# Kernel optimization log

Hardware: AMD Instinct MI355X
Metric: run time of the kernel (lower is better)

Reference implementation:

```python
import jax, jax.numpy as jnp
import numpy as np
import math

LAYER_NUMBER = 2          # coeff for query-key layer scaling
HEAD_DIM = 128
NORM_FACTOR = math.sqrt(HEAD_DIM) * LAYER_NUMBER  # apply_query_key_layer_scaling
COEFF = float(LAYER_NUMBER)
MASK_FILL = -10000.0


def setup_inputs() -> dict:
    key = jax.random.key(0)
    k1, k2, k3, k4 = jax.random.split(key, 4)
    sq, b, nh, hn = 2048, 2, 16, HEAD_DIM
    query_layer = jax.random.normal(k1, (sq, b, nh, hn), dtype=jnp.float32)
    key_layer = jax.random.normal(k2, (sq, b, nh, hn), dtype=jnp.float32)
    value_layer = jax.random.normal(k3, (sq, b, nh, hn), dtype=jnp.float32)
    attention_mask = jax.random.bernoulli(k4, 0.1, (b, 1, sq, sq))
    return {
        "query_layer": query_layer,
        "key_layer": key_layer,
        "value_layer": value_layer,
        "attention_mask": attention_mask,
    }


def reference(query_layer, key_layer, value_layer, attention_mask):
    sq, b, nh, hn = query_layer.shape
    # raw scores: QK^T / norm_factor  -> [b, h, sq, sk]
    scores = jnp.einsum("sbhd,tbhd->bhst", query_layer, key_layer) / NORM_FACTOR
    # MatchedScaleMaskSoftmax: scale by coeff (softmax in fp32), mask-fill, softmax
    x = scores * COEFF
    x = jnp.where(attention_mask, MASK_FILL, x)
    probs = jax.nn.softmax(x, axis=-1)
    # zero out rows where every key is masked
    all_k_masked = jnp.all(attention_mask, axis=-1)  # [b, 1, sq]
    probs = probs * (1.0 - all_k_masked.astype(probs.dtype))[..., None]
    # (dropout p=0.0 -> identity)
    # context: probs @ V -> [sq, b, h, hn] -> [sq, b, hidden]
    ctx = jnp.einsum("bhst,tbhd->sbhd", probs, value_layer)
    return ctx.reshape(sq, b, nh * hn)
```

## Files before the change

kernel.cpp:

```cpp
#include <hip/hip_runtime.h>
#include <math.h>

#define SQ   2048
#define DH   128
#define NKT  32
#define SCALEF 0.08838834764831845f
#define SHIFTF 16.0f

typedef __attribute__((ext_vector_type(8))) short bf16x8;
typedef __attribute__((ext_vector_type(4))) float f32x4;

__device__ __forceinline__ unsigned short f2b(float f) {
    unsigned int u = __float_as_uint(f);
    u += 0x7FFFu + ((u >> 16) & 1u);
    return (unsigned short)(u >> 16);
}

typedef __attribute__((address_space(1))) const unsigned int guint;
typedef __attribute__((address_space(3))) unsigned int luint;
__device__ __forceinline__ void load_lds16(const void* g, void* l) {
    __builtin_amdgcn_global_load_lds((guint*)g, (luint*)l, 16, 0, 0);
}


__global__ __launch_bounds__(256)
void prep_all(const float* __restrict__ K, const float* __restrict__ V,
              const int* __restrict__ M,
              unsigned short* __restrict__ Kp, unsigned short* __restrict__ Vp,
              unsigned long long* __restrict__ B)
{
    const int bid = blockIdx.x;
    const int tid = threadIdx.x;
    if (bid < 4096) {
        int id   = bid * 256 + tid;
        int quad = id & 3;
        int key  = (id >> 2) & 63;
        int ks   = (id >> 8) & 3;
        int kt   = (id >> 10) & 31;
        int bh   = id >> 15;
        const float* src = K + (size_t)(kt * 64 + key) * 4096 + bh * DH + ks * 32 + quad * 8;
        float4 f0 = *(const float4*)src;
        float4 f1 = *(const float4*)(src + 4);
        uint4 o;
        o.x = (unsigned)f2b(f0.x) | ((unsigned)f2b(f0.y) << 16);
        o.y = (unsigned)f2b(f0.z) | ((unsigned)f2b(f0.w) << 16);
        o.z = (unsigned)f2b(f1.x) | ((unsigned)f2b(f1.y) << 16);
        o.w = (unsigned)f2b(f1.z) | ((unsigned)f2b(f1.w) << 16);
        *(uint4*)(Kp + (size_t)id * 8) = o;
    } else if (bid < 5120) {
        int t  = bid - 4096;
        int kt = t & 31, bh = t >> 5;
        int d  = tid & 127;
        int hf = tid >> 7;
        const float* vb = V + (size_t)kt * 64 * 4096 + bh * DH + d;
        unsigned short* ob = Vp + (size_t)t * 8192 + (size_t)(hf * 128 + d) * 32;
        #pragma unroll
        for (int p = 0; p < 4; p++) {
            unsigned short v[8];
            #pragma unroll
            for (int j = 0; j < 8; j++)
                v[j] = f2b(vb[(size_t)(hf * 32 + p * 8 + j) * 4096]);
            uint4 o;
            o.x = (unsigned)v[0] | ((unsigned)v[1] << 16);
            o.y = (unsigned)v[2] | ((unsigned)v[3] << 16);
            o.z = (unsigned)v[4] | ((unsigned)v[5] << 16);
            o.w = (unsigned)v[6] | ((unsigned)v[7] << 16);
            *(uint4*)(ob + p * 8) = o;
        }
    } else {
        int b2   = bid - 5120;
        int wid  = b2 * 4 + (tid >> 6);
        int lane = tid & 63;
        const int* src = M + (size_t)wid * SQ + lane;
        unsigned long long* dst = B + (size_t)wid * NKT;
        for (int t = 0; t < NKT; t++) {
            unsigned long long bm = __ballot(src[t * 64] != 0);
            if (lane == 0) dst[t] = bm;
        }
    }
}

__global__ __launch_bounds__(256, 2)
void fa2(const float* __restrict__ Q, const unsigned short* __restrict__ Kp,
         const unsigned short* __restrict__ Vp, const unsigned long long* __restrict__ MB,
         float* __restrict__ out)
{
    __shared__ __align__(16) unsigned short K_lds[64 * 128];
    __shared__ __align__(16) unsigned short V_lds[64 * 128];
    __shared__ __align__(16) unsigned short P_lds[4 * 2048];

    const int tid  = threadIdx.x;
    const int w    = tid >> 6;
    const int lane = tid & 63;
    const int quad = lane >> 4;
    const int c    = lane & 15;

    const int bid = blockIdx.x;
    const int qt  = bid & 15;
    const int bh  = bid >> 4;
    const int b_i = bh >> 4;
    const int qbase = qt * 128 + w * 32;
    const size_t bh_off = (size_t)bh * DH;

    bf16x8 aq[2][4];
    #pragma unroll
    for (int blk = 0; blk < 2; blk++) {
        const float* qrow = Q + (size_t)(qbase + blk * 16 + c) * 4096 + bh_off;
        #pragma unroll
        for (int ks = 0; ks < 4; ks++) {
            const int d0 = ks * 32 + quad * 8;
            float4 f0 = *(const float4*)(qrow + d0);
            float4 f1 = *(const float4*)(qrow + d0 + 4);
            bf16x8 a;
            a[0] = (short)f2b(f0.x); a[1] = (short)f2b(f0.y);
            a[2] = (short)f2b(f0.z); a[3] = (short)f2b(f0.w);
            a[4] = (short)f2b(f1.x); a[5] = (short)f2b(f1.y);
            a[6] = (short)f2b(f1.z); a[7] = (short)f2b(f1.w);
            aq[blk][ks] = a;
        }
    }

    f32x4 oa[2][8];
    #pragma unroll
    for (int blk = 0; blk < 2; blk++)
        #pragma unroll
        for (int nb = 0; nb < 8; nb++) oa[blk][nb] = (f32x4){0.f, 0.f, 0.f, 0.f};
    float l[2][4];
    #pragma unroll
    for (int blk = 0; blk < 2; blk++)
        #pragma unroll
        for (int r = 0; r < 4; r++) l[blk][r] = 0.0f;

    const unsigned short* KpT = Kp + (size_t)bh * (NKT * 8192);
    const unsigned short* VpT = Vp + (size_t)bh * (NKT * 8192);
    const unsigned long long* mb0 = MB + (size_t)(b_i * SQ + qbase + quad * 4) * NKT;
    const unsigned long long* mb1 = mb0 + 16 * NKT;
    unsigned short* Pw = &P_lds[w * 2048];

    for (int kt = 0; kt < NKT; kt++) {
        __syncthreads();
        {
            const unsigned short* kg = KpT + (size_t)kt * 8192;
            const unsigned short* vg = VpT + (size_t)kt * 8192;
            #pragma unroll
            for (int i = 0; i < 4; i++) {
                int ch = w * 64 + i * 256;
                load_lds16(kg + (size_t)(ch + lane) * 8, &K_lds[ch * 8]);
            }
            #pragma unroll
            for (int i = 0; i < 4; i++) {
                int ch = w * 64 + i * 256;
                load_lds16(vg + (size_t)(ch + lane) * 8, &V_lds[ch * 8]);
            }
        }
        unsigned long long mrow[2][4];
        #pragma unroll
        for (int r = 0; r < 4; r++) {
            mrow[0][r] = mb0[r * NKT + kt];
            mrow[1][r] = mb1[r * NKT + kt];
        }
        __syncthreads();

        f32x4 s[2][4];
        #pragma unroll
        for (int blk = 0; blk < 2; blk++)
            #pragma unroll
            for (int nb = 0; nb < 4; nb++) s[blk][nb] = (f32x4){0.f, 0.f, 0.f, 0.f};
        #pragma unroll
        for (int nb = 0; nb < 4; nb++) {
            bf16x8 bk[4];
            #pragma unroll
            for (int ks = 0; ks < 4; ks++)
                bk[ks] = *(const bf16x8*)&K_lds[ks * 2048 + nb * 512 + c * 32 + quad * 8];
            #pragma unroll
            for (int blk = 0; blk < 2; blk++)
                #pragma unroll
                for (int ks = 0; ks < 4; ks++)
                    s[blk][nb] = __builtin_amdgcn_mfma_f32_16x16x32_bf16(aq[blk][ks], bk[ks], s[blk][nb], 0, 0, 0);
        }

        #pragma unroll
        for (int blk = 0; blk < 2; blk++) {
            #pragma unroll
            for (int r = 0; r < 4; r++) {
                unsigned long long bits = mrow[blk][r];
                #pragma unroll
                for (int nb = 0; nb < 4; nb++) {
                    float p = __expf(fmaf(s[blk][nb][r], SCALEF, -SHIFTF));
                    if ((unsigned)(bits >> (nb * 16 + c)) & 1u) p = 0.0f;
                    l[blk][r] += p;
                    int quad2 = (((nb & 1) * 2) + (c >> 3)) ^ quad;
                    Pw[(nb >> 1) * 1024 + blk * 512 + quad * 128 + r * 32 + quad2 * 8 + (c & 7)] = f2b(p);
                }
            }
        }

        bf16x8 ap[2][2];
        #pragma unroll
        for (int blk = 0; blk < 2; blk++)
            #pragma unroll
            for (int ks2 = 0; ks2 < 2; ks2++)
                ap[blk][ks2] = *(const bf16x8*)&Pw[ks2 * 1024 + blk * 512 + c * 32 + ((quad ^ (c >> 2)) * 8)];
        #pragma unroll
        for (int nb = 0; nb < 8; nb++) {
            bf16x8 bv0 = *(const bf16x8*)&V_lds[nb * 512 + c * 32 + quad * 8];
            bf16x8 bv1 = *(const bf16x8*)&V_lds[4096 + nb * 512 + c * 32 + quad * 8];
            #pragma unroll
            for (int blk = 0; blk < 2; blk++) {
                oa[blk][nb] = __builtin_amdgcn_mfma_f32_16x16x32_bf16(ap[blk][0], bv0, oa[blk][nb], 0, 0, 0);
                oa[blk][nb] = __builtin_amdgcn_mfma_f32_16x16x32_bf16(ap[blk][1], bv1, oa[blk][nb], 0, 0, 0);
            }
        }
    }

    #pragma unroll
    for (int blk = 0; blk < 2; blk++) {
        #pragma unroll
        for (int r = 0; r < 4; r++) {
            float t = l[blk][r];
            t += __shfl_xor(t, 1, 64);
            t += __shfl_xor(t, 2, 64);
            t += __shfl_xor(t, 4, 64);
            t += __shfl_xor(t, 8, 64);
            float inv = (t > 0.0f) ? (1.0f / t) : 0.0f;
            float* orow = out + (size_t)(qbase + blk * 16 + quad * 4 + r) * 4096 + bh_off;
            #pragma unroll
            for (int nb = 0; nb < 8; nb++)
                orow[nb * 16 + c] = oa[blk][nb][r] * inv;
        }
    }
}

__global__ __launch_bounds__(256)
void fa_fallback(const float* __restrict__ Q, const float* __restrict__ K,
                 const float* __restrict__ V, const int* __restrict__ mask,
                 float* __restrict__ out)
{
    __shared__ unsigned short K_lds[64 * 136];
    __shared__ unsigned short Vt_lds[128 * 72];
    __shared__ unsigned short P_lds[4 * 16 * 72];
    const int tid = threadIdx.x, w = tid >> 6, lane = tid & 63, quad = lane >> 4, c = lane & 15;
    const int gid = blockIdx.x, qtile = gid & 31, bh = gid >> 5, b_i = bh >> 4;
    const int q0 = qtile * 64 + w * 16;
    const size_t bh_off = (size_t)bh * DH;
    bf16x8 aq[4];
    {
        const float* qrow = Q + (size_t)(q0 + c) * 4096 + bh_off;
        #pragma unroll
        for (int ks = 0; ks < 4; ks++) {
            const int d0 = ks * 32 + quad * 8;
            float4 f0 = *(const float4*)(qrow + d0);
            float4 f1 = *(const float4*)(qrow + d0 + 4);
            bf16x8 a;
            a[0] = (short)f2b(f0.x); a[1] = (short)f2b(f0.y); a[2] = (short)f2b(f0.z); a[3] = (short)f2b(f0.w);
            a[4] = (short)f2b(f1.x); a[5] = (short)f2b(f1.y); a[6] = (short)f2b(f1.z); a[7] = (short)f2b(f1.w);
            aq[ks] = a;
        }
    }
    float m_i[4], l_i[4];
    #pragma unroll
    for (int r = 0; r < 4; r++) { m_i[r] = -INFINITY; l_i[r] = 0.0f; }
    f32x4 o_acc[8];
    #pragma unroll
    for (int nb = 0; nb < 8; nb++) o_acc[nb] = (f32x4){0.f, 0.f, 0.f, 0.f};
    const int srow = tid >> 2, scol = (tid & 3) * 4;
    const int* mbase = mask + (size_t)b_i * SQ * SQ;
    for (int kt = 0; kt < SQ; kt += 64) {
        __syncthreads();
        {
            const float* krow = K + (size_t)(kt + srow) * 4096 + bh_off;
            const float* vrow = V + (size_t)(kt + srow) * 4096 + bh_off;
            #pragma unroll
            for (int j = 0; j < 8; j++) {
                const int d0 = scol + j * 16;
                float4 kf = *(const float4*)(krow + d0);
                unsigned lo = (unsigned)f2b(kf.x) | ((unsigned)f2b(kf.y) << 16);
                unsigned hi = (unsigned)f2b(kf.z) | ((unsigned)f2b(kf.w) << 16);
                *(uint2*)&K_lds[srow * 136 + d0] = make_uint2(lo, hi);
                float4 vf = *(const float4*)(vrow + d0);
                Vt_lds[(d0 + 0) * 72 + srow] = f2b(vf.x);
                Vt_lds[(d0 + 1) * 72 + srow] = f2b(vf.y);
                Vt_lds[(d0 + 2) * 72 + srow] = f2b(vf.z);
                Vt_lds[(d0 + 3) * 72 + srow] = f2b(vf.w);
            }
        }
        __syncthreads();
        f32x4 s[4];
        #pragma unroll
        for (int nb = 0; nb < 4; nb++) s[nb] = (f32x4){0.f, 0.f, 0.f, 0.f};
        #pragma unroll
        for (int nb = 0; nb < 4; nb++)
            #pragma unroll
            for (int ks = 0; ks < 4; ks++) {
                bf16x8 bk = *(const bf16x8*)&K_lds[(nb * 16 + c) * 136 + ks * 32 + quad * 8];
                s[nb] = __builtin_amdgcn_mfma_f32_16x16x32_bf16(aq[ks], bk, s[nb], 0, 0, 0);
            }
        float rowmax[4];
        #pragma unroll
        for (int r = 0; r < 4; r++) rowmax[r] = -INFINITY;
        #pragma unroll
        for (int r = 0; r < 4; r++) {
            const int* mp = mbase + (size_t)(q0 + quad * 4 + r) * SQ + kt + c;
            #pragma unroll
            for (int nb = 0; nb < 4; nb++) {
                float v = s[nb][r] * SCALEF;
                if (mp[nb * 16] != 0) v = -10000.0f;
                s[nb][r] = v;
                rowmax[r] = fmaxf(rowmax[r], v);
            }
        }
        #pragma unroll
        for (int r = 0; r < 4; r++)
            #pragma unroll
            for (int off = 1; off < 16; off <<= 1)
                rowmax[r] = fmaxf(rowmax[r], __shfl_xor(rowmax[r], off, 64));
        float alpha[4], rowsum[4];
        #pragma unroll
        for (int r = 0; r < 4; r++) {
            float mn = fmaxf(m_i[r], rowmax[r]);
            alpha[r] = __expf(m_i[r] - mn);
            m_i[r] = mn;
            rowsum[r] = 0.0f;
        }
        #pragma unroll
        for (int r = 0; r < 4; r++)
            #pragma unroll
            for (int nb = 0; nb < 4; nb++) {
                float p = __expf(s[nb][r] - m_i[r]);
                rowsum[r] += p;
                P_lds[(w * 16 + quad * 4 + r) * 72 + nb * 16 + c] = f2b(p);
            }
        #pragma unroll
        for (int r = 0; r < 4; r++) {
            #pragma unroll
            for (int off = 1; off < 16; off <<= 1)
                rowsum[r] += __shfl_xor(rowsum[r], off, 64);
            l_i[r] = l_i[r] * alpha[r] + rowsum[r];
        }
        #pragma unroll
        for (int nb = 0; nb < 8; nb++)
            #pragma unroll
            for (int r = 0; r < 4; r++) o_acc[nb][r] *= alpha[r];
        bf16x8 ap[2];
        #pragma unroll
        for (int ks = 0; ks < 2; ks++)
            ap[ks] = *(const bf16x8*)&P_lds[(w * 16 + c) * 72 + ks * 32 + quad * 8];
        #pragma unroll
        for (int nb = 0; nb < 8; nb++)
            #pragma unroll
            for (int ks = 0; ks < 2; ks++) {
                bf16x8 bv = *(const bf16x8*)&Vt_lds[(nb * 16 + c) * 72 + ks * 32 + quad * 8];
                o_acc[nb] = __builtin_amdgcn_mfma_f32_16x16x32_bf16(ap[ks], bv, o_acc[nb], 0, 0, 0);
            }
    }
    float inv[4];
    #pragma unroll
    for (int r = 0; r < 4; r++) inv[r] = (m_i[r] > -9999.0f) ? (1.0f / l_i[r]) : 0.0f;
    #pragma unroll
    for (int r = 0; r < 4; r++) {
        float* orow = out + (size_t)(q0 + quad * 4 + r) * 4096 + bh_off;
        #pragma unroll
        for (int nb = 0; nb < 8; nb++) orow[nb * 16 + c] = o_acc[nb][r] * inv[r];
    }
}

extern "C" void kernel_launch(void* const* d_in, const int* in_sizes, int n_in,
                              void* d_out, int out_size, void* d_ws, size_t ws_size,
                              hipStream_t stream) {
    const float* Q    = (const float*)d_in[0];
    const float* K    = (const float*)d_in[1];
    const float* V    = (const float*)d_in[2];
    const int*   mask = (const int*)d_in[3];
    float* out = (float*)d_out;

    const size_t KP_BYTES = (size_t)32 * 32 * 8192 * 2;
    const size_t NEED = 2 * KP_BYTES + (size_t)4096 * NKT * 8;
    if (ws_size < NEED) {
        fa_fallback<<<dim3(1024), dim3(256), 0, stream>>>(Q, K, V, mask, out);
        return;
    }
    unsigned short* Kp = (unsigned short*)d_ws;
    unsigned short* Vp = (unsigned short*)((char*)d_ws + KP_BYTES);
    unsigned long long* MB = (unsigned long long*)((char*)d_ws + 2 * KP_BYTES);

    prep_all<<<dim3(6144), dim3(256), 0, stream>>>(K, V, mask, Kp, Vp, MB);
    fa2<<<dim3(512), dim3(256), 0, stream>>>(Q, Kp, Vp, MB, out);
}
```

Baseline: 280.0 us.

## Double-buffer K/V tiles in LDS, use hardware bf16 pack and exp2, split prep kernels

```diff
diff --git a/kernel.cpp b/kernel.cpp
--- a/kernel.cpp
+++ b/kernel.cpp
@@ -4,8 +4,9 @@
 #define SQ   2048
 #define DH   128
 #define NKT  32
-#define SCALEF 0.08838834764831845f
-#define SHIFTF 16.0f
+#define SCALEF  0.08838834764831845f
+#define SCALE2  0.12751743f
+#define NSHIFT2 (-23.083121f)
 
 typedef __attribute__((ext_vector_type(8))) short bf16x8;
 typedef __attribute__((ext_vector_type(4))) float f32x4;
@@ -15,6 +16,16 @@
     u += 0x7FFFu + ((u >> 16) & 1u);
     return (unsigned short)(u >> 16);
 }
+__device__ __forceinline__ unsigned int cvtpk(float lo, float hi) {
+    unsigned int r;
+    asm("v_cvt_pk_bf16_f32 %0, %1, %2" : "=v"(r) : "v"(lo), "v"(hi));
+    return r;
+}
+__device__ __forceinline__ float fexp2(float x) {
+    float r;
+    asm("v_exp_f32 %0, %1" : "=v"(r) : "v"(x));
+    return r;
+}
 
 typedef __attribute__((address_space(1))) const unsigned int guint;
 typedef __attribute__((address_space(3))) unsigned int luint;
@@ -24,69 +35,146 @@
 
 
 __global__ __launch_bounds__(256)
-void prep_all(const float* __restrict__ K, const float* __restrict__ V,
-              const int* __restrict__ M,
-              unsigned short* __restrict__ Kp, unsigned short* __restrict__ Vp,
-              unsigned long long* __restrict__ B)
+void prep_k(const float* __restrict__ K, unsigned short* __restrict__ Kp)
 {
-    const int bid = blockIdx.x;
-    const int tid = threadIdx.x;
-    if (bid < 4096) {
-        int id   = bid * 256 + tid;
-        int quad = id & 3;
-        int key  = (id >> 2) & 63;
-        int ks   = (id >> 8) & 3;
-        int kt   = (id >> 10) & 31;
-        int bh   = id >> 15;
-        const float* src = K + (size_t)(kt * 64 + key) * 4096 + bh * DH + ks * 32 + quad * 8;
-        float4 f0 = *(const float4*)src;
-        float4 f1 = *(const float4*)(src + 4);
+    int id   = blockIdx.x * 256 + threadIdx.x;
+    int quad = id & 3;
+    int key  = (id >> 2) & 63;
+    int ks   = (id >> 8) & 3;
+    int kt   = (id >> 10) & 31;
+    int bh   = id >> 15;
+    const float* src = K + (size_t)(kt * 64 + key) * 4096 + bh * DH + ks * 32 + quad * 8;
+    float4 f0 = *(const float4*)src;
+    float4 f1 = *(const float4*)(src + 4);
+    uint4 o;
+    o.x = cvtpk(f0.x, f0.y); o.y = cvtpk(f0.z, f0.w);
+    o.z = cvtpk(f1.x, f1.y); o.w = cvtpk(f1.z, f1.w);
+    *(uint4*)(Kp + (size_t)id * 8) = o;
+}
+
+__global__ __launch_bounds__(512)
+void prep_v(const float* __restrict__ V, unsigned short* __restrict__ Vp)
+{
+    int t    = blockIdx.x;
+    int kt   = t & 31, bh = t >> 5;
+    int quad = threadIdx.x & 3;
+    int d    = threadIdx.x >> 2;
+    const float* vb = V + (size_t)(kt * 64) * 4096 + bh * DH + d;
+    unsigned short* ob = Vp + (size_t)t * 8192;
+    #pragma unroll
+    for (int ks2 = 0; ks2 < 2; ks2++) {
+        float f[8];
+        #pragma unroll
+        for (int j = 0; j < 8; j++)
+            f[j] = vb[(size_t)(ks2 * 32 + quad * 8 + j) * 4096];
         uint4 o;
-        o.x = (unsigned)f2b(f0.x) | ((unsigned)f2b(f0.y) << 16);
-        o.y = (unsigned)f2b(f0.z) | ((unsigned)f2b(f0.w) << 16);
-        o.z = (unsigned)f2b(f1.x) | ((unsigned)f2b(f1.y) << 16);
-        o.w = (unsigned)f2b(f1.z) | ((unsigned)f2b(f1.w) << 16);
-        *(uint4*)(Kp + (size_t)id * 8) = o;
-    } else if (bid < 5120) {
-        int t  = bid - 4096;
-        int kt = t & 31, bh = t >> 5;
-        int d  = tid & 127;
-        int hf = tid >> 7;
-        const float* vb = V + (size_t)kt * 64 * 4096 + bh * DH + d;
-        unsigned short* ob = Vp + (size_t)t * 8192 + (size_t)(hf * 128 + d) * 32;
-        #pragma unroll
-        for (int p = 0; p < 4; p++) {
-            unsigned short v[8];
-            #pragma unroll
-            for (int j = 0; j < 8; j++)
-                v[j] = f2b(vb[(size_t)(hf * 32 + p * 8 + j) * 4096]);
-            uint4 o;
-            o.x = (unsigned)v[0] | ((unsigned)v[1] << 16);
-            o.y = (unsigned)v[2] | ((unsigned)v[3] << 16);
-            o.z = (unsigned)v[4] | ((unsigned)v[5] << 16);
-            o.w = (unsigned)v[6] | ((unsigned)v[7] << 16);
-            *(uint4*)(ob + p * 8) = o;
-        }
-    } else {
-        int b2   = bid - 5120;
-        int wid  = b2 * 4 + (tid >> 6);
-        int lane = tid & 63;
-        const int* src = M + (size_t)wid * SQ + lane;
-        unsigned long long* dst = B + (size_t)wid * NKT;
-        for (int t = 0; t < NKT; t++) {
-            unsigned long long bm = __ballot(src[t * 64] != 0);
-            if (lane == 0) dst[t] = bm;
-        }
-    }
-}
+        o.x = cvtpk(f[0], f[1]); o.y = cvtpk(f[2], f[3]);
+        o.z = cvtpk(f[4], f[5]); o.w = cvtpk(f[6], f[7]);
+        *(uint4*)(ob + ((size_t)(ks2 * 128 + d) * 4 + quad) * 8) = o;
+    }
+}
+
+__global__ __launch_bounds__(256)
+void prep_m(const int* __restrict__ M, unsigned long long* __restrict__ B)
+{
+    int wid  = blockIdx.x * 4 + (threadIdx.x >> 6);
+    int lane = threadIdx.x & 63;
+    const int* src = M + (size_t)wid * SQ + lane;
+    unsigned long long* dst = B + (size_t)wid * NKT;
+    #pragma unroll
+    for (int t = 0; t < NKT; t++) {
+        unsigned long long bm = __ballot(src[t * 64] != 0);
+        if (lane == 0) dst[t] = bm;
+    }
+}
+
+#define STAGE(Kl, Vl, ktt) do {                                              \
+    const unsigned short* kg_ = KpT + (size_t)(ktt) * 8192;                  \
+    const unsigned short* vg_ = VpT + (size_t)(ktt) * 8192;                  \
+    _Pragma("unroll") for (int i_ = 0; i_ < 4; i_++) {                       \
+        int ch_ = w * 64 + i_ * 256;                                         \
+        load_lds16(kg_ + (size_t)(ch_ + lane) * 8, &Kl[ch_ * 8]);            \
+    }                                                                        \
+    _Pragma("unroll") for (int i_ = 0; i_ < 4; i_++) {                       \
+        int ch_ = w * 64 + i_ * 256;                                         \
+        load_lds16(vg_ + (size_t)(ch_ + lane) * 8, &Vl[ch_ * 8]);            \
+    }                                                                        \
+} while (0)
+
+#define LOADMR(mr, ktt) do {                                                 \
+    _Pragma("unroll") for (int r_ = 0; r_ < 4; r_++) {                       \
+        mr[0][r_] = mb0[r_ * NKT + (ktt)];                                   \
+        mr[1][r_] = mb1[r_ * NKT + (ktt)];                                   \
+    }                                                                        \
+} while (0)
+
+#define COMPUTE(Kl, Vl, mr) do {                                             \
+    f32x4 s[2][4];                                                           \
+    _Pragma("unroll") for (int blk = 0; blk < 2; blk++)                      \
+        _Pragma("unroll") for (int nb = 0; nb < 4; nb++)                     \
+            s[blk][nb] = (f32x4){0.f, 0.f, 0.f, 0.f};                        \
+    __builtin_amdgcn_s_setprio(1);                                           \
+    _Pragma("unroll") for (int nb = 0; nb < 4; nb++) {                       \
+        bf16x8 bk[4];                                                        \
+        _Pragma("unroll") for (int ks = 0; ks < 4; ks++)                     \
+            bk[ks] = *(const bf16x8*)&Kl[ks * 2048 + nb * 512 + c * 32 + quad * 8]; \
+        _Pragma("unroll") for (int blk = 0; blk < 2; blk++)                  \
+            _Pragma("unroll") for (int ks = 0; ks < 4; ks++)                 \
+                s[blk][nb] = __builtin_amdgcn_mfma_f32_16x16x32_bf16(aq[blk][ks], bk[ks], s[blk][nb], 0, 0, 0); \
+    }                                                                        \
+    __builtin_amdgcn_s_setprio(0);                                           \
+    _Pragma("unroll") for (int blk = 0; blk < 2; blk++) {                    \
+        _Pragma("unroll") for (int r = 0; r < 4; r++) {                      \
+            unsigned long long bits = mr[blk][r];                            \
+            unsigned wlo = (unsigned)(bits >> c);                            \
+            unsigned whi = (unsigned)(bits >> 32) >> c;                      \
+            _Pragma("unroll") for (int nbp = 0; nbp < 2; nbp++) {            \
+                unsigned wb = nbp ? whi : wlo;                               \
+                float p0 = fexp2(fmaf(s[blk][2 * nbp][r],     SCALE2, NSHIFT2)); \
+                float p1 = fexp2(fmaf(s[blk][2 * nbp + 1][r], SCALE2, NSHIFT2)); \
+                if (wb & 1u)       p0 = 0.0f;                                \
+                if (wb & 0x10000u) p1 = 0.0f;                                \
+                l[blk][r] += p0 + p1;                                        \
+                unsigned pk = cvtpk(p0, p1);                                 \
+                int base = nbp * 1024 + blk * 512 + quad * 128 + r * 32 + (c & 7); \
+                Pw[base + ((0 + (c >> 3)) ^ quad) * 8] = (unsigned short)pk; \
+                Pw[base + ((2 + (c >> 3)) ^ quad) * 8] = (unsigned short)(pk >> 16); \
+            }                                                                \
+        }                                                                    \
+    }                                                                        \
+    bf16x8 ap[2][2];                                                         \
+    _Pragma("unroll") for (int blk = 0; blk < 2; blk++)                      \
+        _Pragma("unroll") for (int ks2 = 0; ks2 < 2; ks2++)                  \
+            ap[blk][ks2] = *(const bf16x8*)&Pw[ks2 * 1024 + blk * 512 + c * 32 + ((quad ^ (c >> 2)) * 8)]; \
+    __builtin_amdgcn_s_setprio(1);                                           \
+    _Pragma("unroll") for (int nb = 0; nb < 8; nb++) {                       \
+        bf16x8 bv0 = *(const bf16x8*)&Vl[nb * 512 + c * 32 + quad * 8];      \
+        bf16x8 bv1 = *(const bf16x8*)&Vl[4096 + nb * 512 + c * 32 + quad * 8]; \
+        _Pragma("unroll") for (int blk = 0; blk < 2; blk++) {                \
+            oa[blk][nb] = __builtin_amdgcn_mfma_f32_16x16x32_bf16(ap[blk][0], bv0, oa[blk][nb], 0, 0, 0); \
+            oa[blk][nb] = __builtin_amdgcn_mfma_f32_16x16x32_bf16(ap[blk][1], bv1, oa[blk][nb], 0, 0, 0); \
+        }                                                                    \
+    }                                                                        \
+    __builtin_amdgcn_s_setprio(0);                                           \
+} while (0)
+
+#define PIPE_STEP(Kc, Vc, mrC, Kn, Vn, mrN, ktn) do {                        \
+    __builtin_amdgcn_s_barrier();                                            \
+    STAGE(Kn, Vn, (ktn));                                                    \
+    LOADMR(mrN, (ktn));                                                      \
+    asm volatile("s_waitcnt vmcnt(16)" ::: "memory");                        \
+    __builtin_amdgcn_s_barrier();                                            \
+    __builtin_amdgcn_sched_barrier(0);                                       \
+    COMPUTE(Kc, Vc, mrC);                                                    \
+} while (0)
 
 __global__ __launch_bounds__(256, 2)
 void fa2(const float* __restrict__ Q, const unsigned short* __restrict__ Kp,
          const unsigned short* __restrict__ Vp, const unsigned long long* __restrict__ MB,
          float* __restrict__ out)
 {
-    __shared__ __align__(16) unsigned short K_lds[64 * 128];
-    __shared__ __align__(16) unsigned short V_lds[64 * 128];
+    __shared__ __align__(16) unsigned short K_lds[2][64 * 128];
+    __shared__ __align__(16) unsigned short V_lds[2][64 * 128];
     __shared__ __align__(16) unsigned short P_lds[4 * 2048];
 
     const int tid  = threadIdx.x;
@@ -95,7 +183,8 @@
     const int quad = lane >> 4;
     const int c    = lane & 15;
 
-    const int bid = blockIdx.x;
+    const int bid0 = blockIdx.x;
+    const int bid  = ((bid0 & 7) << 6) | (bid0 >> 3);
     const int qt  = bid & 15;
     const int bh  = bid >> 4;
     const int b_i = bh >> 4;
@@ -111,12 +200,10 @@
             const int d0 = ks * 32 + quad * 8;
             float4 f0 = *(const float4*)(qrow + d0);
             float4 f1 = *(const float4*)(qrow + d0 + 4);
-            bf16x8 a;
-            a[0] = (short)f2b(f0.x); a[1] = (short)f2b(f0.y);
-            a[2] = (short)f2b(f0.z); a[3] = (short)f2b(f0.w);
-            a[4] = (short)f2b(f1.x); a[5] = (short)f2b(f1.y);
-            a[6] = (short)f2b(f1.z); a[7] = (short)f2b(f1.w);
-            aq[blk][ks] = a;
+            uint4 u;
+            u.x = cvtpk(f0.x, f0.y); u.y = cvtpk(f0.z, f0.w);
+            u.z = cvtpk(f1.x, f1.y); u.w = cvtpk(f1.z, f1.w);
+            aq[blk][ks] = *(bf16x8*)&u;
         }
     }
 
@@ -137,81 +224,16 @@
     const unsigned long long* mb1 = mb0 + 16 * NKT;
     unsigned short* Pw = &P_lds[w * 2048];
 
-    for (int kt = 0; kt < NKT; kt++) {
-        __syncthreads();
-        {
-            const unsigned short* kg = KpT + (size_t)kt * 8192;
-            const unsigned short* vg = VpT + (size_t)kt * 8192;
-            #pragma unroll
-            for (int i = 0; i < 4; i++) {
-                int ch = w * 64 + i * 256;
-                load_lds16(kg + (size_t)(ch + lane) * 8, &K_lds[ch * 8]);
-            }
-            #pragma unroll
-            for (int i = 0; i < 4; i++) {
-                int ch = w * 64 + i * 256;
-                load_lds16(vg + (size_t)(ch + lane) * 8, &V_lds[ch * 8]);
-            }
-        }
-        unsigned long long mrow[2][4];
-        #pragma unroll
-        for (int r = 0; r < 4; r++) {
-            mrow[0][r] = mb0[r * NKT + kt];
-            mrow[1][r] = mb1[r * NKT + kt];
-        }
-        __syncthreads();
-
-        f32x4 s[2][4];
-        #pragma unroll
-        for (int blk = 0; blk < 2; blk++)
-            #pragma unroll
-            for (int nb = 0; nb < 4; nb++) s[blk][nb] = (f32x4){0.f, 0.f, 0.f, 0.f};
-        #pragma unroll
-        for (int nb = 0; nb < 4; nb++) {
-            bf16x8 bk[4];
-            #pragma unroll
-            for (int ks = 0; ks < 4; ks++)
-                bk[ks] = *(const bf16x8*)&K_lds[ks * 2048 + nb * 512 + c * 32 + quad * 8];
-            #pragma unroll
-            for (int blk = 0; blk < 2; blk++)
-                #pragma unroll
-                for (int ks = 0; ks < 4; ks++)
-                    s[blk][nb] = __builtin_amdgcn_mfma_f32_16x16x32_bf16(aq[blk][ks], bk[ks], s[blk][nb], 0, 0, 0);
-        }
-
-        #pragma unroll
-        for (int blk = 0; blk < 2; blk++) {
-            #pragma unroll
-            for (int r = 0; r < 4; r++) {
-                unsigned long long bits = mrow[blk][r];
-                #pragma unroll
-                for (int nb = 0; nb < 4; nb++) {
-                    float p = __expf(fmaf(s[blk][nb][r], SCALEF, -SHIFTF));
-                    if ((unsigned)(bits >> (nb * 16 + c)) & 1u) p = 0.0f;
-                    l[blk][r] += p;
-                    int quad2 = (((nb & 1) * 2) + (c >> 3)) ^ quad;
-                    Pw[(nb >> 1) * 1024 + blk * 512 + quad * 128 + r * 32 + quad2 * 8 + (c & 7)] = f2b(p);
-                }
-            }
-        }
-
-        bf16x8 ap[2][2];
-        #pragma unroll
-        for (int blk = 0; blk < 2; blk++)
-            #pragma unroll
-            for (int ks2 = 0; ks2 < 2; ks2++)
-                ap[blk][ks2] = *(const bf16x8*)&Pw[ks2 * 1024 + blk * 512 + c * 32 + ((quad ^ (c >> 2)) * 8)];
-        #pragma unroll
-        for (int nb = 0; nb < 8; nb++) {
-            bf16x8 bv0 = *(const bf16x8*)&V_lds[nb * 512 + c * 32 + quad * 8];
-            bf16x8 bv1 = *(const bf16x8*)&V_lds[4096 + nb * 512 + c * 32 + quad * 8];
-            #pragma unroll
-            for (int blk = 0; blk < 2; blk++) {
-                oa[blk][nb] = __builtin_amdgcn_mfma_f32_16x16x32_bf16(ap[blk][0], bv0, oa[blk][nb], 0, 0, 0);
-                oa[blk][nb] = __builtin_amdgcn_mfma_f32_16x16x32_bf16(ap[blk][1], bv1, oa[blk][nb], 0, 0, 0);
-            }
-        }
-    }
+    unsigned long long mrA[2][4], mrB[2][4];
+
+    STAGE(K_lds[0], V_lds[0], 0);
+    LOADMR(mrA, 0);
+
+    for (int kt = 0; kt < NKT; kt += 2) {
+        PIPE_STEP(K_lds[0], V_lds[0], mrA, K_lds[1], V_lds[1], mrB, kt + 1);
+        PIPE_STEP(K_lds[1], V_lds[1], mrB, K_lds[0], V_lds[0], mrA, (kt + 2) & 31);
+    }
+    asm volatile("s_waitcnt vmcnt(0)" ::: "memory");
 
     #pragma unroll
     for (int blk = 0; blk < 2; blk++) {
@@ -383,6 +405,8 @@
     unsigned short* Vp = (unsigned short*)((char*)d_ws + KP_BYTES);
     unsigned long long* MB = (unsigned long long*)((char*)d_ws + 2 * KP_BYTES);
 
-    prep_all<<<dim3(6144), dim3(256), 0, stream>>>(K, V, mask, Kp, Vp, MB);
+    prep_k<<<dim3(4096), dim3(256), 0, stream>>>(K, Kp);
+    prep_v<<<dim3(1024), dim3(512), 0, stream>>>(V, Vp);
+    prep_m<<<dim3(1024), dim3(256), 0, stream>>>(mask, MB);
     fa2<<<dim3(512), dim3(256), 0, stream>>>(Q, Kp, Vp, MB, out);
 }
```

Measured after the change: 271.8 us. -2.9%, faster.
